# Performance work log

Measured on AMD Instinct MI355X. Metric: run time of the kernel, lower is better.

Reference implementation:

```python
import jax, jax.numpy as jnp
import numpy as np

K, T, RHO, V, TH, EH, S, B = 50, 50, 300, 20000, 800, 200, 10, 256
DELTA = 0.005
LOG_DELTA = float(np.log(DELTA))
EPS = 1e-6


def setup_inputs() -> dict:
    key = jax.random.key(0)
    ks = jax.random.split(key, 32)
    f32 = jnp.float32
    rn = lambda i, shp, s=0.02: jax.random.normal(ks[i], shp, f32) * s
    inp = {
        "unique_tokens": jax.random.randint(ks[0], (100,), 0, V),
        "bows": jax.random.uniform(ks[1], (B, V), f32),
        "normalized_bows": jax.random.uniform(ks[2], (B, V), f32),
        "times": jax.random.randint(ks[3], (B,), 0, T),
        "sources": jax.random.randint(ks[4], (B,), 0, S),
        "rnn_inp": jax.random.normal(ks[5], (S, T, V), f32),
        "num_docs": 100000,
        # learned parameters
        "mu_q_alpha": rn(6, (K, T, RHO), 1.0),
        "logsigma_q_alpha": rn(7, (K, T, RHO), 0.1),
        "rho_W": rn(8, (V, RHO)),                 # Linear(rho_size -> vocab, no bias)
        "W1": rn(9, (TH, V + K)), "b1": jnp.zeros((TH,), f32),
        "W2": rn(10, (TH, TH)), "b2": jnp.zeros((TH,), f32),
        "mu_th_W": rn(11, (K, TH)), "mu_th_b": jnp.zeros((K,), f32),
        "ls_th_W": rn(12, (K, TH)), "ls_th_b": jnp.zeros((K,), f32),
        "eta_map_W": rn(13, (EH, V)), "eta_map_b": jnp.zeros((EH,), f32),
        "lstm_Wih": rn(14, (4 * EH, EH)), "lstm_Whh": rn(15, (4 * EH, EH)),
        "lstm_bih": jnp.zeros((4 * EH,), f32), "lstm_bhh": jnp.zeros((4 * EH,), f32),
        "mu_eta_W": rn(16, (K, EH + K)), "mu_eta_b": jnp.zeros((K,), f32),
        "ls_eta_W": rn(17, (K, EH + K)), "ls_eta_b": jnp.zeros((K,), f32),
        "cls_W": rn(18, (S, K)), "cls_b": jnp.zeros((S,), f32),
    }
    return inp


def _lstm(x_seq, Wih, Whh, bih, bhh):
    # x_seq: [T, S, EH]; torch gate order i,f,g,o
    def step(carry, x):
        h, c = carry
        z = x @ Wih.T + bih + h @ Whh.T + bhh
        i, f, g, o = jnp.split(z, 4, axis=-1)
        c = jax.nn.sigmoid(f) * c + jax.nn.sigmoid(i) * jnp.tanh(g)
        h = jax.nn.sigmoid(o) * jnp.tanh(c)
        return (h, c), h
    h0 = jnp.zeros((x_seq.shape[1], Whh.shape[1]), x_seq.dtype)
    _, out = jax.lax.scan(step, (h0, h0), x_seq)
    return out  # [T, S, EH]


def reference(unique_tokens, bows, normalized_bows, times, sources, rnn_inp, num_docs,
              mu_q_alpha, logsigma_q_alpha, rho_W, W1, b1, W2, b2,
              mu_th_W, mu_th_b, ls_th_W, ls_th_b, eta_map_W, eta_map_b,
              lstm_Wih, lstm_Whh, lstm_bih, lstm_bhh,
              mu_eta_W, mu_eta_b, ls_eta_W, ls_eta_b, cls_W, cls_b):
    # eval-mode semantics: reparameterize returns mu, dropout off
    bsz = bows.shape[0]
    coeff = num_docs / bsz

    # ---- alpha: eval-mode alphas_t == mu_q_alpha[:, t, :]; KL vectorized ----
    mu_a, ls_a = mu_q_alpha, logsigma_q_alpha  # [K, T, RHO]
    kl_a0 = 0.5 * jnp.sum((jnp.exp(ls_a[:, 0]) + mu_a[:, 0] ** 2) / (1.0 + EPS) - 1.0 - ls_a[:, 0])
    diff = mu_a[:, 1:] - mu_a[:, :-1]
    kl_at = 0.5 * jnp.sum((jnp.exp(ls_a[:, 1:]) + diff ** 2) / (DELTA + EPS) - 1.0 + LOG_DELTA - ls_a[:, 1:])
    kl_alpha = kl_a0 + kl_at
    alphas = jnp.transpose(mu_a, (1, 0, 2))  # [T, K, RHO]

    # ---- eta: LSTM over time (vmapped over sources as batch), then recurrence ----
    mapped = jnp.einsum('stv,hv->sth', rnn_inp, eta_map_W) + eta_map_b  # [S, T, EH]
    lstm_out = _lstm(jnp.transpose(mapped, (1, 0, 2)), lstm_Wih, lstm_Whh, lstm_bih, lstm_bhh)  # [T, S, EH]

    inp0 = jnp.concatenate([lstm_out[0], jnp.zeros((S, K), lstm_out.dtype)], axis=-1)
    mu0 = inp0 @ mu_eta_W.T + mu_eta_b
    ls0 = inp0 @ ls_eta_W.T + ls_eta_b  # no clipping at t=0 in original
    kl0 = 0.5 * jnp.sum((jnp.exp(ls0) + mu0 ** 2) / (1.0 + EPS) - 1.0 - ls0)

    def eta_step(carry, out_t):
        eta_prev, kl = carry
        inp_t = jnp.concatenate([out_t, eta_prev], axis=-1)
        mu_t = inp_t @ mu_eta_W.T + mu_eta_b
        ls_t = jnp.clip(inp_t @ ls_eta_W.T + ls_eta_b, -10.0, 10.0)
        kl_t = 0.5 * jnp.sum((jnp.exp(ls_t) + (mu_t - eta_prev) ** 2) / (DELTA + EPS) - 1.0 + LOG_DELTA - ls_t)
        return (mu_t, kl + kl_t), mu_t
    (_, kl_rest), etas_rest = jax.lax.scan(eta_step, (mu0, jnp.float32(0.0)), lstm_out[1:])
    etas = jnp.transpose(jnp.concatenate([mu0[None], etas_rest], axis=0), (1, 0, 2))  # [S, T, K]
    kl_eta = kl0 + kl_rest

    # ---- theta ----
    eta_std = etas[sources, times]  # [B, K]
    h = jax.nn.relu(jnp.concatenate([normalized_bows, eta_std], axis=1) @ W1.T + b1)
    h = jax.nn.relu(h @ W2.T + b2)
    mu_t = h @ mu_th_W.T + mu_th_b
    ls_t = jnp.clip(h @ ls_th_W.T + ls_th_b, -10.0, 10.0)
    theta = jax.nn.softmax(mu_t, axis=-1)
    kl_theta = (0.5 * jnp.sum((jnp.exp(ls_t) + (mu_t - eta_std) ** 2) / (1.0 + EPS) - 1.0 - ls_t)) * coeff

    # ---- beta and NLL ----
    logit = jnp.einsum('tkr,vr->tkv', alphas, rho_W)
    beta = jax.nn.softmax(logit, axis=-1)        # [T, K, V]
    beta_d = beta[times]                         # [B, K, V]
    loglik = jnp.log(jnp.einsum('bk,bkv->bv', theta, beta_d))
    nll = -jnp.sum(loglik * bows) * coeff

    # ---- source prediction loss (sum-reduced cross entropy) ----
    logits = theta @ cls_W.T + cls_b
    logp = jax.nn.log_softmax(logits, axis=-1)
    pred_loss = -jnp.sum(jnp.take_along_axis(logp, sources[:, None], axis=1)) * coeff

    nelbo = nll + kl_alpha + kl_eta + kl_theta + pred_loss
    return (nelbo, nll, kl_alpha, kl_eta, kl_theta, pred_loss)
```

## Files before the change

kernel.cpp:

```cpp
#include <hip/hip_runtime.h>

typedef unsigned int u32;
typedef unsigned short ushort_t;

#define NTOP 50
#define NT_T 50
#define NRHO 300
#define NVOC 20000
#define NTH 800
#define NEH 200
#define NSRC 10
#define NBAT 256

#define OFF_SCAL     0
#define OFF_MAPPED   16
#define OFF_HPRE     100016
#define OFF_H2       304816
#define OFF_Z        509616
#define OFF_DOCCNT   512120
#define OFF_DOCLIST  512176
#define MEMSET_BYTES ((size_t)524976 * 4)
#define OFF_XW       524976
#define OFF_BIAS2    924976
#define OFF_ETAS     925776
#define OFF_WCOEF    950776
#define OFF_W1E      963576
#define OFF_WHH_H    1003576
#define OFF_ETAWH    1083576
#define OFF_H1B      1096080
#define OFF_MAPB     1198480
#define OFF_WIHB     1255824
#define OFF_W2B      1356176
#define OFF_ALPHAB   1714576
#define OFF_RHOB     2124176
#define OFF_NBB      5339536
#define OFF_W1B      7899536
#define OFF_RNNB     16859536
#define OFF_EMWB     21979536
#define OFF_LOGITH   7899536

typedef _Float16 h2v __attribute__((ext_vector_type(2)));
typedef __bf16 bf16x8 __attribute__((ext_vector_type(8)));
typedef float f32x4 __attribute__((ext_vector_type(4)));

__device__ inline float dot2u(u32 a, u32 b, float c){
  h2v ha = __builtin_bit_cast(h2v, a), hb = __builtin_bit_cast(h2v, b);
#if __has_builtin(__builtin_amdgcn_fdot2)
  return __builtin_amdgcn_fdot2(ha, hb, c, false);
#else
  return c + (float)ha.x*(float)hb.x + (float)ha.y*(float)hb.y;
#endif
}

__device__ inline u32 packh2(float lo, float hi){
  h2v h; h.x = (_Float16)lo; h.y = (_Float16)hi;
  return __builtin_bit_cast(u32, h);
}

__device__ inline ushort_t f2bf(float f){
  u32 u = __builtin_bit_cast(u32, f);
  u = (u + 0x7FFFu + ((u >> 16) & 1u)) >> 16;
  return (ushort_t)u;
}

__device__ inline float fast_sig(float x){ return 1.f/(1.f + __expf(-x)); }
__device__ inline float fast_tanh(float x){ float e = __expf(2.f*x); return 1.f - 2.f/(e + 1.f); }

__device__ __forceinline__ void gl2lds16(const void* g, void* l){
  __builtin_amdgcn_global_load_lds((__attribute__((address_space(1))) void*)g,
                                   (__attribute__((address_space(3))) void*)l,
                                   16, 0, 0);
}

__device__ inline void blockReduceAdd(float v, float* red, float* target){
  int tid = threadIdx.x;
  red[tid] = v; __syncthreads();
  for (int o = blockDim.x >> 1; o > 0; o >>= 1){
    if (tid < o) red[tid] += red[tid + o];
    __syncthreads();
  }
  if (tid == 0) atomicAdd(target, red[0]);
}

__global__ __launch_bounds__(256) void k_prep(
    const float* __restrict__ whh,
    const float* __restrict__ muEW, const float* __restrict__ lsEW,
    const float* __restrict__ bih, const float* __restrict__ bhh,
    const float* __restrict__ wih, const float* __restrict__ emapB,
    const float* __restrict__ W1, const int* __restrict__ times,
    float* __restrict__ W)
{
  int idx = blockIdx.x*256 + threadIdx.x;
  u32* whhH = (u32*)(W + OFF_WHH_H);
  u32* etaWH = (u32*)(W + OFF_ETAWH);
  float* bias2 = W + OFF_BIAS2;
  float* w1e = W + OFF_W1E;
  int* docCnt = (int*)(W + OFF_DOCCNT);
  int* docList = (int*)(W + OFF_DOCLIST);
  if (idx < 80000){
    int j = idx/100; int i = idx - j*100;
    whhH[idx] = packh2(whh[j*200 + 2*i], whh[j*200 + 2*i + 1]);
  } else if (idx < 92500){
    int d = idx - 80000; int q = d/125; int i = d - q*125;
    const float* src = (q < 50) ? (muEW + q*250) : (lsEW + (q-50)*250);
    etaWH[d] = packh2(src[2*i], src[2*i+1]);
  } else if (idx < 93300){
    int j = idx - 92500;
    float acc = bih[j] + bhh[j];
    const float* wr = wih + (size_t)j*200;
    #pragma unroll 4
    for (int k = 0; k < 200; k++) acc += emapB[k]*wr[k];
    bias2[j] = acc;
  } else if (idx < 133300){
    int d = idx - 93300; int j = d/50; int k = d - j*50;
    w1e[d] = W1[(size_t)j*20050 + 20000 + k];
  } else if (idx < 133556){
    int b = idx - 133300; int t = times[b];
    int pos = atomicAdd(&docCnt[t], 1);
    docList[t*256 + pos] = b;
  }
}

__global__ __launch_bounds__(256) void k_conv(const float* __restrict__ src, int ldsrc,
                                              int Mreal, int Kused,
                                              ushort_t* __restrict__ dst, int Mp, int Kp)
{
  int idx = blockIdx.x*256 + threadIdx.x;
  int kb = Kp >> 3;
  if (idx >= Mp*kb) return;
  int row = idx / kb, c = (idx - row*kb) << 3;
  ushort_t out[8];
  #pragma unroll
  for (int j = 0; j < 8; j++){
    float v = 0.f;
    int k = c + j;
    if (row < Mreal && k < Kused) v = src[(size_t)row*ldsrc + k];
    out[j] = f2bf(v);
  }
  *(uint4*)(dst + (size_t)row*Kp + c) = *(uint4*)out;
}

__global__ __launch_bounds__(256) void k_conva(const float* __restrict__ muq, ushort_t* __restrict__ dst)
{
  int idx = blockIdx.x*256 + threadIdx.x;
  if (idx >= 2560*40) return;
  int row = idx / 40, c = (idx - row*40) << 3;
  ushort_t out[8];
  const float* src = nullptr;
  if (row < 2500){ int t = row/50, k = row - t*50; src = muq + (size_t)k*15000 + t*300; }
  #pragma unroll
  for (int j = 0; j < 8; j++){
    int r = c + j;
    float v = (src && r < 300) ? src[r] : 0.f;
    out[j] = f2bf(v);
  }
  *(uint4*)(dst + (size_t)row*320 + c) = *(uint4*)out;
}

template<int MODE>
__global__ __launch_bounds__(256) void mfma_nt(
    const ushort_t* __restrict__ A, int lda,
    const ushort_t* __restrict__ B, int ldb,
    float* __restrict__ C, _Float16* __restrict__ Ch, int ldc,
    const float* __restrict__ nBias,
    int M, int N, int mT, int kS, int chunks)
{
  __shared__ __align__(16) ushort_t As[128*32];
  __shared__ __align__(16) ushort_t Bs[128*32];
  int bid = blockIdx.x;
  int kIdx = bid % kS; int rest = bid / kS;
  int mIdx = rest % mT; int nIdx = rest / mT;
  int tid = threadIdx.x;
  int w = tid >> 6, l = tid & 63;
  int c0 = (int)(((long long)chunks * kIdx) / kS);
  int c1 = (int)(((long long)chunks * (kIdx+1)) / kS);
  int r0 = w*32;
  const ushort_t* ga0 = A + (size_t)(mIdx*128 + r0      + (l>>2))*lda + (l&3)*8;
  const ushort_t* ga1 = A + (size_t)(mIdx*128 + r0 + 16 + (l>>2))*lda + (l&3)*8;
  const ushort_t* gb0 = B + (size_t)(nIdx*128 + r0      + (l>>2))*ldb + (l&3)*8;
  const ushort_t* gb1 = B + (size_t)(nIdx*128 + r0 + 16 + (l>>2))*ldb + (l&3)*8;
  ushort_t* la = As + r0*32;
  ushort_t* lb = Bs + r0*32;
  int wr = (w >> 1)*64, wc = (w & 1)*64;
  int lr = l & 15, lq = l >> 4;
  f32x4 acc[4][4];
  #pragma unroll
  for (int i = 0; i < 4; i++)
    #pragma unroll
    for (int j = 0; j < 4; j++)
      acc[i][j] = (f32x4)0.f;

  for (int c = c0; c < c1; c++){
    size_t ko = (size_t)c * 32;
    gl2lds16(ga0 + ko, la);
    gl2lds16(ga1 + ko, la + 512);
    gl2lds16(gb0 + ko, lb);
    gl2lds16(gb1 + ko, lb + 512);
    __syncthreads();
    bf16x8 av[4], bv[4];
    #pragma unroll
    for (int i = 0; i < 4; i++)
      av[i] = *(const bf16x8*)(As + (wr + i*16 + lr)*32 + lq*8);
    #pragma unroll
    for (int j = 0; j < 4; j++)
      bv[j] = *(const bf16x8*)(Bs + (wc + j*16 + lr)*32 + lq*8);
    #pragma unroll
    for (int i = 0; i < 4; i++)
      #pragma unroll
      for (int j = 0; j < 4; j++)
        acc[i][j] = __builtin_amdgcn_mfma_f32_16x16x32_bf16(av[i], bv[j], acc[i][j], 0, 0, 0);
    __syncthreads();
  }
  if (MODE == 3){
    float* Z = C;
    #pragma unroll
    for (int i = 0; i < 4; i++){
      #pragma unroll
      for (int r = 0; r < 4; r++){
        int row = mIdx*128 + wr + i*16 + lq*4 + r;
        float p = 0.f;
        if (row < M){
          #pragma unroll
          for (int j = 0; j < 4; j++){
            int col = nIdx*128 + wc + j*16 + lr;
            if (col < N){
              float e = __expf(acc[i][j][r]);
              Ch[(size_t)row*ldc + col] = (_Float16)e;
              p += e;
            }
          }
        }
        p += __shfl_xor(p, 1, 16);
        p += __shfl_xor(p, 2, 16);
        p += __shfl_xor(p, 4, 16);
        p += __shfl_xor(p, 8, 16);
        if (lr == 0 && row < M) atomicAdd(&Z[row], p);
      }
    }
  } else {
    #pragma unroll
    for (int i = 0; i < 4; i++){
      #pragma unroll
      for (int r = 0; r < 4; r++){
        int row = mIdx*128 + wr + i*16 + lq*4 + r;
        if (row >= M) continue;
        #pragma unroll
        for (int j = 0; j < 4; j++){
          int col = nIdx*128 + wc + j*16 + lr;
          if (col >= N) continue;
          float v = acc[i][j][r];
          if (MODE == 0)      atomicAdd(&C[(size_t)row*ldc + col], v);
          else                C[(size_t)row*ldc + col] = v + nBias[col];
        }
      }
    }
  }
}

__global__ __launch_bounds__(256) void k_klalpha(const float* __restrict__ muq,
                                                 const float* __restrict__ lsq,
                                                 float* __restrict__ W)
{
  __shared__ float red[256];
  const float inv_dl = 1.f/(0.005f + 1e-6f);
  const float logdl = -5.2983173665480363f;
  float local = 0.f;
  for (int idx = blockIdx.x*256 + threadIdx.x; idx < 750000; idx += gridDim.x*256){
    int rem = idx % 15000; int t = rem / 300;
    float ls = lsq[idx]; float mu = muq[idx];
    if (t == 0){
      local += 0.5f*((__expf(ls) + mu*mu)/(1.f + 1e-6f) - 1.f - ls);
    } else {
      float d = mu - muq[idx - 300];
      local += 0.5f*((__expf(ls) + d*d)*inv_dl - 1.f + logdl - ls);
    }
  }
  blockReduceAdd(local, red, W + OFF_SCAL + 1);
}

__global__ __launch_bounds__(512, 2) void k_lstm(
    const float* __restrict__ xw, const u32* __restrict__ whhH, const u32* __restrict__ etaWH,
    const float* __restrict__ muEB, const float* __restrict__ lsEB,
    float* __restrict__ etas, float* __restrict__ W)
{
  int s = blockIdx.x; int tid = threadIdx.x;
  __shared__ uint4 hp4[32];
  __shared__ float zbuf[800];
  __shared__ float red[512];
  u32 wreg[200];
  #pragma unroll
  for (int i = 0; i < 200; i++) wreg[i] = 0u;
  if (tid < 400){
    const u32* ra = whhH + tid*100;
    const u32* rb = whhH + (tid + 400)*100;
    #pragma unroll
    for (int i = 0; i < 100; i++){ wreg[i] = ra[i]; wreg[100+i] = rb[i]; }
  } else if (tid < 500){
    int q = tid - 400;
    const u32* re = etaWH + q*125;
    #pragma unroll
    for (int i = 0; i < 125; i++) wreg[i] = re[i];
  }
  float ebias = 0.f;
  if (tid >= 400 && tid < 500){
    int q = tid - 400;
    ebias = (q < 50) ? muEB[q] : lsEB[q - 50];
  }
  float creg = 0.f, muPrev = 0.f, klLocal = 0.f;
  if (tid < 32){ uint4 z; z.x=z.y=z.z=z.w=0u; hp4[tid] = z; }
  __syncthreads();
  const float inv_dl = 1.f/(0.005f + 1e-6f);
  const float logdl = -5.2983173665480363f;
  _Float16* hview = (_Float16*)hp4;

  for (int t = 0; t < NT_T; t++){
    if (tid < 400){
      float a0=0.f,a1=0.f,a2=0.f,a3=0.f,b0=0.f,b1=0.f,b2=0.f,b3=0.f;
      #pragma unroll
      for (int i4 = 0; i4 < 25; i4++){
        uint4 h = hp4[i4];
        a0 = dot2u(wreg[i4*4+0], h.x, a0);
        a1 = dot2u(wreg[i4*4+1], h.y, a1);
        a2 = dot2u(wreg[i4*4+2], h.z, a2);
        a3 = dot2u(wreg[i4*4+3], h.w, a3);
        b0 = dot2u(wreg[100+i4*4+0], h.x, b0);
        b1 = dot2u(wreg[100+i4*4+1], h.y, b1);
        b2 = dot2u(wreg[100+i4*4+2], h.z, b2);
        b3 = dot2u(wreg[100+i4*4+3], h.w, b3);
      }
      const float* xr = xw + (size_t)(s*50 + t)*800;
      zbuf[tid]       = ((a0+a1)+(a2+a3)) + xr[tid];
      zbuf[tid + 400] = ((b0+b1)+(b2+b3)) + xr[tid + 400];
    }
    __syncthreads();
    if (tid < 200){
      float zi = zbuf[tid], zf = zbuf[200+tid], zg = zbuf[400+tid], zo = zbuf[600+tid];
      float ig = fast_sig(zi);
      float fg = fast_sig(zf);
      float gg = fast_tanh(zg);
      float og = fast_sig(zo);
      creg = fg*creg + ig*gg;
      float hv = og*fast_tanh(creg);
      hview[tid] = (_Float16)hv;
    }
    __syncthreads();
    float eacc = 0.f;
    bool isEta = (tid >= 400 && tid < 500);
    if (isEta){
      float e0=ebias, e1=0.f, e2=0.f, e3=0.f;
      #pragma unroll
      for (int i4 = 0; i4 < 32; i4++){
        uint4 h = hp4[i4];
        e0 = dot2u(wreg[i4*4+0], h.x, e0);
        e1 = dot2u(wreg[i4*4+1], h.y, e1);
        e2 = dot2u(wreg[i4*4+2], h.z, e2);
        e3 = dot2u(wreg[i4*4+3], h.w, e3);
      }
      eacc = (e0+e1)+(e2+e3);
    }
    __syncthreads();
    if (isEta){
      int q = tid - 400;
      if (q < 50){
        float mu = eacc;
        etas[(size_t)(s*50 + t)*50 + q] = mu;
        if (t == 0) klLocal += 0.5f*mu*mu/(1.f + 1e-6f);
        else { float d = mu - muPrev; klLocal += 0.5f*d*d*inv_dl; }
        muPrev = mu;
        hview[200 + q] = (_Float16)mu;
      } else {
        float ls = eacc;
        if (t == 0) klLocal += 0.5f*(__expf(ls)/(1.f + 1e-6f) - 1.f - ls);
        else {
          ls = fminf(fmaxf(ls, -10.f), 10.f);
          klLocal += 0.5f*(__expf(ls)*inv_dl - 1.f + logdl - ls);
        }
      }
    }
  }
  __syncthreads();
  blockReduceAdd(klLocal, red, W + OFF_SCAL + 2);
}

__global__ __launch_bounds__(256) void k_h1(
    const float* __restrict__ hpre, const float* __restrict__ b1, const float* __restrict__ w1e,
    const float* __restrict__ etas, const int* __restrict__ times, const int* __restrict__ srcs,
    ushort_t* __restrict__ h1B)
{
  int b = blockIdx.x, tid = threadIdx.x;
  __shared__ float et[50];
  int tb = times[b], sb = srcs[b];
  if (tid < 50) et[tid] = etas[(size_t)(sb*50 + tb)*50 + tid];
  __syncthreads();
  for (int j = tid; j < 800; j += 256){
    float acc = hpre[(size_t)b*800 + j] + b1[j];
    const float* wrow = w1e + (size_t)j*50;
    #pragma unroll
    for (int k = 0; k < 50; k++) acc += et[k]*wrow[k];
    h1B[(size_t)b*800 + j] = f2bf(fmaxf(acc, 0.f));
  }
}

__global__ __launch_bounds__(256) void k_thfin(
    const float* __restrict__ h2g, const float* __restrict__ b2, const float* __restrict__ etas,
    const int* __restrict__ times, const int* __restrict__ srcs,
    const float* __restrict__ muW, const float* __restrict__ muB,
    const float* __restrict__ lsW, const float* __restrict__ lsB,
    const float* __restrict__ clsW, const float* __restrict__ clsB,
    const float* __restrict__ Zrow, float* __restrict__ wcoef, float* __restrict__ W)
{
  int b = blockIdx.x, tid = threadIdx.x;
  __shared__ float h2s[800], mu[50], lsv[50], et[50], th[50], lg[10], red[64], shm[2];
  for (int j = tid; j < 800; j += 256) h2s[j] = fmaxf(h2g[(size_t)b*800 + j] + b2[j], 0.f);
  int tb = times[b], sb = srcs[b];
  if (tid < 50) et[tid] = etas[(size_t)(sb*50 + tb)*50 + tid];
  __syncthreads();
  if (tid < 100){
    int q = (tid < 50) ? tid : tid - 50;
    const float* w = (tid < 50) ? (muW + (size_t)q*800) : (lsW + (size_t)q*800);
    float acc = (tid < 50) ? muB[q] : lsB[q];
    #pragma unroll 8
    for (int j = 0; j < 800; j++) acc += h2s[j]*w[j];
    if (tid < 50) mu[q] = acc;
    else lsv[q] = fminf(fmaxf(acc, -10.f), 10.f);
  }
  __syncthreads();
  if (tid == 0){ float m = -1e30f; for (int k = 0; k < 50; k++) m = fmaxf(m, mu[k]); shm[0] = m; }
  __syncthreads();
  if (tid < 50) th[tid] = __expf(mu[tid] - shm[0]);
  __syncthreads();
  if (tid == 0){ float z = 0.f; for (int k = 0; k < 50; k++) z += th[k]; shm[1] = z; }
  __syncthreads();
  if (tid < 64) red[tid] = 0.f;
  if (tid < 50){
    float t_ = th[tid]/shm[1]; th[tid] = t_;
    wcoef[(size_t)b*50 + tid] = t_/Zrow[tb*50 + tid];
    float d = mu[tid] - et[tid];
    red[tid] = 0.5f*((__expf(lsv[tid]) + d*d)/(1.f + 1e-6f) - 1.f - lsv[tid]);
  }
  __syncthreads();
  if (tid < 10){
    float a = clsB[tid];
    #pragma unroll
    for (int k = 0; k < 50; k++) a += th[k]*clsW[tid*50 + k];
    lg[tid] = a;
  }
  __syncthreads();
  if (tid == 0){
    float m = -1e30f; for (int i = 0; i < 10; i++) m = fmaxf(m, lg[i]);
    float z = 0.f; for (int i = 0; i < 10; i++) z += __expf(lg[i] - m);
    float lse = m + __logf(z);
    atomicAdd(W + OFF_SCAL + 4, lse - lg[sb]);
    float ssum = 0.f; for (int i = 0; i < 50; i++) ssum += red[i];
    atomicAdd(W + OFF_SCAL + 3, ssum);
  }
}

__global__ __launch_bounds__(256) void k_nll(
    const _Float16* __restrict__ E, const float* __restrict__ wcoef,
    const float* __restrict__ bows, float* __restrict__ W)
{
  int t = blockIdx.x/10, vc = blockIdx.x%10;
  int v0 = vc*2000;
  int tid = threadIdx.x;
  const int* docCnt = (const int*)(W + OFF_DOCCNT);
  const int* docList = (const int*)(W + OFF_DOCLIST);
  __shared__ float wch[64*50];
  __shared__ int ids[64];
  __shared__ float red[256];
  int nd = docCnt[t];
  float acc = 0.f;
  for (int d0 = 0; d0 < nd; d0 += 64){
    int ndc = min(64, nd - d0);
    __syncthreads();
    for (int i = tid; i < ndc*50; i += 256){
      int d = i/50, k = i - d*50;
      int bb = docList[t*256 + d0 + d];
      if (k == 0) ids[d] = bb;
      wch[i] = wcoef[(size_t)bb*50 + k];
    }
    __syncthreads();
    for (int v = v0 + tid; v < v0 + 2000; v += 256){
      float e[50];
      #pragma unroll
      for (int k = 0; k < 50; k++)
        e[k] = (float)E[(size_t)(t*50 + k)*NVOC + v];
      for (int d = 0; d < ndc; d++){
        float s = 0.f;
        #pragma unroll
        for (int k = 0; k < 50; k++) s += wch[d*50 + k]*e[k];
        acc += bows[(size_t)ids[d]*NVOC + v]*__logf(s);
      }
    }
  }
  __syncthreads();
  blockReduceAdd(acc, red, W + OFF_SCAL + 0);
}

__global__ void k_final(const float* __restrict__ W, const int* __restrict__ ndocs, float* __restrict__ out)
{
  if (blockIdx.x == 0 && threadIdx.x == 0){
    float coeff = (float)ndocs[0] / 256.f;
    const float* scal = W + OFF_SCAL;
    float nll  = -scal[0]*coeff;
    float kla  = scal[1];
    float kle  = scal[2];
    float klth = scal[3]*coeff;
    float pred = scal[4]*coeff;
    out[0] = nll + kla + kle + klth + pred;
    out[1] = nll; out[2] = kla; out[3] = kle; out[4] = klth; out[5] = pred;
  }
}

extern "C" void kernel_launch(void* const* d_in, const int* in_sizes, int n_in,
                              void* d_out, int out_size, void* d_ws, size_t ws_size,
                              hipStream_t stream)
{
  (void)in_sizes; (void)n_in; (void)out_size; (void)ws_size;
  const float* bows  = (const float*)d_in[1];
  const float* nb    = (const float*)d_in[2];
  const int*   times = (const int*)d_in[3];
  const int*   srcs  = (const int*)d_in[4];
  const float* rnn   = (const float*)d_in[5];
  const int*   ndocs = (const int*)d_in[6];
  const float* muq   = (const float*)d_in[7];
  const float* lsq   = (const float*)d_in[8];
  const float* rho   = (const float*)d_in[9];
  const float* W1    = (const float*)d_in[10];
  const float* b1    = (const float*)d_in[11];
  const float* W2    = (const float*)d_in[12];
  const float* b2    = (const float*)d_in[13];
  const float* muthW = (const float*)d_in[14];
  const float* muthB = (const float*)d_in[15];
  const float* lsthW = (const float*)d_in[16];
  const float* lsthB = (const float*)d_in[17];
  const float* emapW = (const float*)d_in[18];
  const float* emapB = (const float*)d_in[19];
  const float* wih   = (const float*)d_in[20];
  const float* whh   = (const float*)d_in[21];
  const float* bih   = (const float*)d_in[22];
  const float* bhh   = (const float*)d_in[23];
  const float* muEW  = (const float*)d_in[24];
  const float* muEB  = (const float*)d_in[25];
  const float* lsEW  = (const float*)d_in[26];
  const float* lsEB  = (const float*)d_in[27];
  const float* clsW  = (const float*)d_in[28];
  const float* clsB  = (const float*)d_in[29];

  float* W = (float*)d_ws;
  ushort_t* alphaB = (ushort_t*)(W + OFF_ALPHAB);
  ushort_t* rhoB   = (ushort_t*)(W + OFF_RHOB);
  ushort_t* nbB    = (ushort_t*)(W + OFF_NBB);
  ushort_t* w1B    = (ushort_t*)(W + OFF_W1B);
  ushort_t* rnnB   = (ushort_t*)(W + OFF_RNNB);
  ushort_t* emwB   = (ushort_t*)(W + OFF_EMWB);
  ushort_t* wihB   = (ushort_t*)(W + OFF_WIHB);
  ushort_t* w2B    = (ushort_t*)(W + OFF_W2B);
  ushort_t* mapB   = (ushort_t*)(W + OFF_MAPB);
  ushort_t* h1B    = (ushort_t*)(W + OFF_H1B);
  _Float16* Ehalf  = (_Float16*)(W + OFF_LOGITH);

  hipMemsetAsync(d_ws, 0, MEMSET_BYTES, stream);

  k_prep<<<522, 256, 0, stream>>>(whh, muEW, lsEW, bih, bhh, wih, emapB, W1, times, W);

  k_conva<<<400, 256, 0, stream>>>(muq, alphaB);
  k_conv<<<3140, 256, 0, stream>>>(rho, 300, 20000, 300, rhoB, 20096, 320);
  k_conv<<<2500, 256, 0, stream>>>(nb, 20000, 256, 20000, nbB, 256, 20000);
  k_conv<<<8750, 256, 0, stream>>>(W1, 20050, 800, 20000, w1B, 896, 20000);
  k_conv<<<5000, 256, 0, stream>>>(rnn, 20000, 500, 20000, rnnB, 512, 20000);
  k_conv<<<2500, 256, 0, stream>>>(emapW, 20000, 200, 20000, emwB, 256, 20000);
  k_conv<<<98, 256, 0, stream>>>(wih, 200, 800, 200, wihB, 896, 224);
  k_conv<<<350, 256, 0, stream>>>(W2, 800, 800, 800, w2B, 896, 800);

  mfma_nt<0><<<4*2*32, 256, 0, stream>>>(
      rnnB, 20000, emwB, 20000, W + OFF_MAPPED, nullptr, 200, nullptr,
      500, 200, 4, 32, 625);

  mfma_nt<0><<<2*7*20, 256, 0, stream>>>(
      nbB, 20000, w1B, 20000, W + OFF_HPRE, nullptr, 800, nullptr,
      256, 800, 2, 20, 625);

  mfma_nt<3><<<20*157, 256, 0, stream>>>(
      alphaB, 320, rhoB, 320, W + OFF_Z, Ehalf, 20000, nullptr,
      2500, 20000, 20, 1, 10);

  k_conv<<<56, 256, 0, stream>>>(W + OFF_MAPPED, 200, 500, 200, mapB, 512, 224);

  mfma_nt<2><<<4*7, 256, 0, stream>>>(
      mapB, 224, wihB, 224, W + OFF_XW, nullptr, 800, W + OFF_BIAS2,
      500, 800, 4, 1, 7);

  k_klalpha<<<1024, 256, 0, stream>>>(muq, lsq, W);

  k_lstm<<<NSRC, 512, 0, stream>>>(W + OFF_XW, (const u32*)(W + OFF_WHH_H),
                                   (const u32*)(W + OFF_ETAWH), muEB, lsEB,
                                   W + OFF_ETAS, W);

  k_h1<<<256, 256, 0, stream>>>(W + OFF_HPRE, b1, W + OFF_W1E, W + OFF_ETAS, times, srcs, h1B);

  mfma_nt<0><<<2*7*2, 256, 0, stream>>>(
      h1B, 800, w2B, 800, W + OFF_H2, nullptr, 800, nullptr,
      256, 800, 2, 2, 25);

  k_thfin<<<256, 256, 0, stream>>>(W + OFF_H2, b2, W + OFF_ETAS, times, srcs,
                                   muthW, muthB, lsthW, lsthB, clsW, clsB,
                                   W + OFF_Z, W + OFF_WCOEF, W);

  k_nll<<<500, 256, 0, stream>>>(Ehalf, W + OFF_WCOEF, bows, W);

  k_final<<<1, 64, 0, stream>>>(W, ndocs, (float*)d_out);
}
```

Measured before the change: 733.9 us.

## Fuse prep, conversion and KL-alpha kernels into one launch; double-buffer LSTM hidden state

Merges the prep, all bf16 conversion kernels and the KL-alpha reduction into a single large kernel that dispatches work by block index, replacing ten launches with one. The LSTM now keeps its weights in named uint4 registers instead of an indexed array, and pads the eta weights to 128 entries per row so they can be loaded as uint4. It also double-buffers the hidden-state shared buffer, which removes one __syncthreads per timestep because the eta projection reads the new h and the previous eta half from separate buffers. The risks are higher register pressure and a heavier branchy mega-kernel.

```diff
diff --git a/kernel.cpp b/kernel.cpp
--- a/kernel.cpp
+++ b/kernel.cpp
@@ -27,21 +27,25 @@
 #define OFF_W1E      963576
 #define OFF_WHH_H    1003576
 #define OFF_ETAWH    1083576
-#define OFF_H1B      1096080
-#define OFF_MAPB     1198480
-#define OFF_WIHB     1255824
-#define OFF_W2B      1356176
-#define OFF_ALPHAB   1714576
-#define OFF_RHOB     2124176
-#define OFF_NBB      5339536
-#define OFF_W1B      7899536
-#define OFF_RNNB     16859536
-#define OFF_EMWB     21979536
-#define OFF_LOGITH   7899536
+#define OFF_H1B      1096376
+#define OFF_MAPB     1198776
+#define OFF_WIHB     1256120
+#define OFF_W2B      1356472
+#define OFF_ALPHAB   1714872
+#define OFF_RHOB     2124472
+#define OFF_NBB      5339832
+#define OFF_W1B      7899832
+#define OFF_RNNB     16859832
+#define OFF_EMWB     21979832
+#define OFF_LOGITH   7899832
 
 typedef _Float16 h2v __attribute__((ext_vector_type(2)));
 typedef __bf16 bf16x8 __attribute__((ext_vector_type(8)));
 typedef float f32x4 __attribute__((ext_vector_type(4)));
+
+#define REP25(M) M(0) M(1) M(2) M(3) M(4) M(5) M(6) M(7) M(8) M(9) M(10) M(11) M(12) \
+                 M(13) M(14) M(15) M(16) M(17) M(18) M(19) M(20) M(21) M(22) M(23) M(24)
+#define REP7(M) M(0) M(1) M(2) M(3) M(4) M(5) M(6)
 
 __device__ inline float dot2u(u32 a, u32 b, float c){
   h2v ha = __builtin_bit_cast(h2v, a), hb = __builtin_bit_cast(h2v, b);
@@ -82,52 +86,11 @@
   if (tid == 0) atomicAdd(target, red[0]);
 }
 
-__global__ __launch_bounds__(256) void k_prep(
-    const float* __restrict__ whh,
-    const float* __restrict__ muEW, const float* __restrict__ lsEW,
-    const float* __restrict__ bih, const float* __restrict__ bhh,
-    const float* __restrict__ wih, const float* __restrict__ emapB,
-    const float* __restrict__ W1, const int* __restrict__ times,
-    float* __restrict__ W)
-{
-  int idx = blockIdx.x*256 + threadIdx.x;
-  u32* whhH = (u32*)(W + OFF_WHH_H);
-  u32* etaWH = (u32*)(W + OFF_ETAWH);
-  float* bias2 = W + OFF_BIAS2;
-  float* w1e = W + OFF_W1E;
-  int* docCnt = (int*)(W + OFF_DOCCNT);
-  int* docList = (int*)(W + OFF_DOCLIST);
-  if (idx < 80000){
-    int j = idx/100; int i = idx - j*100;
-    whhH[idx] = packh2(whh[j*200 + 2*i], whh[j*200 + 2*i + 1]);
-  } else if (idx < 92500){
-    int d = idx - 80000; int q = d/125; int i = d - q*125;
-    const float* src = (q < 50) ? (muEW + q*250) : (lsEW + (q-50)*250);
-    etaWH[d] = packh2(src[2*i], src[2*i+1]);
-  } else if (idx < 93300){
-    int j = idx - 92500;
-    float acc = bih[j] + bhh[j];
-    const float* wr = wih + (size_t)j*200;
-    #pragma unroll 4
-    for (int k = 0; k < 200; k++) acc += emapB[k]*wr[k];
-    bias2[j] = acc;
-  } else if (idx < 133300){
-    int d = idx - 93300; int j = d/50; int k = d - j*50;
-    w1e[d] = W1[(size_t)j*20050 + 20000 + k];
-  } else if (idx < 133556){
-    int b = idx - 133300; int t = times[b];
-    int pos = atomicAdd(&docCnt[t], 1);
-    docList[t*256 + pos] = b;
-  }
-}
-
-__global__ __launch_bounds__(256) void k_conv(const float* __restrict__ src, int ldsrc,
-                                              int Mreal, int Kused,
-                                              ushort_t* __restrict__ dst, int Mp, int Kp)
-{
-  int idx = blockIdx.x*256 + threadIdx.x;
+__device__ inline void conv_seg(const float* __restrict__ src, int ldsrc,
+                                int Mreal, int Kused,
+                                ushort_t* __restrict__ dst, int Kp, int idx)
+{
   int kb = Kp >> 3;
-  if (idx >= Mp*kb) return;
   int row = idx / kb, c = (idx - row*kb) << 3;
   ushort_t out[8];
   #pragma unroll
@@ -140,21 +103,104 @@
   *(uint4*)(dst + (size_t)row*Kp + c) = *(uint4*)out;
 }
 
-__global__ __launch_bounds__(256) void k_conva(const float* __restrict__ muq, ushort_t* __restrict__ dst)
+__global__ __launch_bounds__(256) void k_mega(
+    const float* __restrict__ whh,
+    const float* __restrict__ muEW, const float* __restrict__ lsEW,
+    const float* __restrict__ bih, const float* __restrict__ bhh,
+    const float* __restrict__ wih, const float* __restrict__ emapB,
+    const float* __restrict__ W1, const int* __restrict__ times,
+    const float* __restrict__ muq, const float* __restrict__ lsq,
+    const float* __restrict__ rho, const float* __restrict__ nb,
+    const float* __restrict__ rnn, const float* __restrict__ emapW,
+    const float* __restrict__ W2f, float* __restrict__ W)
+{
+  int b = blockIdx.x, tid = threadIdx.x;
+  __shared__ float red[256];
+  if (b < 523){
+    int idx = b*256 + tid;
+    u32* whhH = (u32*)(W + OFF_WHH_H);
+    u32* etaWH = (u32*)(W + OFF_ETAWH);
+    if (idx < 80000){
+      int j = idx/100; int i = idx - j*100;
+      whhH[idx] = packh2(whh[j*200 + 2*i], whh[j*200 + 2*i + 1]);
+    } else if (idx < 92800){
+      int d = idx - 80000; int q = d >> 7; int i = d & 127;
+      u32 v = 0u;
+      if (i < 125){
+        const float* src = (q < 50) ? (muEW + q*250) : (lsEW + (q-50)*250);
+        v = packh2(src[2*i], src[2*i+1]);
+      }
+      etaWH[d] = v;
+    } else if (idx < 93600){
+      int j = idx - 92800;
+      float acc = bih[j] + bhh[j];
+      const float* wr = wih + (size_t)j*200;
+      #pragma unroll 4
+      for (int k = 0; k < 200; k++) acc += emapB[k]*wr[k];
+      W[OFF_BIAS2 + j] = acc;
+    } else if (idx < 133600){
+      int d = idx - 93600; int j = d/50; int k = d - j*50;
+      W[OFF_W1E + d] = W1[(size_t)j*20050 + 20000 + k];
+    } else if (idx < 133856){
+      int bb = idx - 133600; int t = times[bb];
+      int* docCnt = (int*)(W + OFF_DOCCNT);
+      int* docList = (int*)(W + OFF_DOCLIST);
+      int pos = atomicAdd(&docCnt[t], 1);
+      docList[t*256 + pos] = bb;
+    }
+  } else if (b < 923){
+    int idx = (b-523)*256 + tid;
+    int row = idx / 40, c = (idx - row*40) << 3;
+    ushort_t out[8];
+    const float* src = nullptr;
+    if (row < 2500){ int t = row/50, k = row - t*50; src = muq + (size_t)k*15000 + t*300; }
+    #pragma unroll
+    for (int j = 0; j < 8; j++){
+      int r = c + j;
+      float v = (src && r < 300) ? src[r] : 0.f;
+      out[j] = f2bf(v);
+    }
+    *(uint4*)((ushort_t*)(W + OFF_ALPHAB) + (size_t)row*320 + c) = *(uint4*)out;
+  } else if (b < 4063){
+    conv_seg(rho, 300, 20000, 300, (ushort_t*)(W + OFF_RHOB), 320, (b-923)*256 + tid);
+  } else if (b < 6563){
+    conv_seg(nb, 20000, 256, 20000, (ushort_t*)(W + OFF_NBB), 20000, (b-4063)*256 + tid);
+  } else if (b < 15313){
+    conv_seg(W1, 20050, 800, 20000, (ushort_t*)(W + OFF_W1B), 20000, (b-6563)*256 + tid);
+  } else if (b < 20313){
+    conv_seg(rnn, 20000, 500, 20000, (ushort_t*)(W + OFF_RNNB), 20000, (b-15313)*256 + tid);
+  } else if (b < 22813){
+    conv_seg(emapW, 20000, 200, 20000, (ushort_t*)(W + OFF_EMWB), 20000, (b-20313)*256 + tid);
+  } else if (b < 22911){
+    conv_seg(wih, 200, 800, 200, (ushort_t*)(W + OFF_WIHB), 224, (b-22813)*256 + tid);
+  } else if (b < 23261){
+    conv_seg(W2f, 800, 800, 800, (ushort_t*)(W + OFF_W2B), 800, (b-22911)*256 + tid);
+  } else {
+    const float inv_dl = 1.f/(0.005f + 1e-6f);
+    const float logdl = -5.2983173665480363f;
+    float local = 0.f;
+    for (int idx = (b-23261)*256 + tid; idx < 750000; idx += 1024*256){
+      int rem = idx % 15000; int t = rem / 300;
+      float ls = lsq[idx]; float mu = muq[idx];
+      if (t == 0){
+        local += 0.5f*((__expf(ls) + mu*mu)/(1.f + 1e-6f) - 1.f - ls);
+      } else {
+        float d = mu - muq[idx - 300];
+        local += 0.5f*((__expf(ls) + d*d)*inv_dl - 1.f + logdl - ls);
+      }
+    }
+    blockReduceAdd(local, red, W + OFF_SCAL + 1);
+  }
+}
+
+__global__ __launch_bounds__(256) void k_conv(const float* __restrict__ src, int ldsrc,
+                                              int Mreal, int Kused,
+                                              ushort_t* __restrict__ dst, int Mp, int Kp)
 {
   int idx = blockIdx.x*256 + threadIdx.x;
-  if (idx >= 2560*40) return;
-  int row = idx / 40, c = (idx - row*40) << 3;
-  ushort_t out[8];
-  const float* src = nullptr;
-  if (row < 2500){ int t = row/50, k = row - t*50; src = muq + (size_t)k*15000 + t*300; }
-  #pragma unroll
-  for (int j = 0; j < 8; j++){
-    int r = c + j;
-    float v = (src && r < 300) ? src[r] : 0.f;
-    out[j] = f2bf(v);
-  }
-  *(uint4*)(dst + (size_t)row*320 + c) = *(uint4*)out;
+  int kb = Kp >> 3;
+  if (idx >= Mp*kb) return;
+  conv_seg(src, ldsrc, Mreal, Kused, dst, Kp, idx);
 }
 
 template<int MODE>
@@ -257,77 +303,55 @@
   }
 }
 
-__global__ __launch_bounds__(256) void k_klalpha(const float* __restrict__ muq,
-                                                 const float* __restrict__ lsq,
-                                                 float* __restrict__ W)
-{
-  __shared__ float red[256];
+__global__ __launch_bounds__(512, 2) void k_lstm(
+    const float* __restrict__ xw, const u32* __restrict__ whhH, const uint4* __restrict__ etaW4,
+    const float* __restrict__ muEB, const float* __restrict__ lsEB,
+    float* __restrict__ etas, float* __restrict__ W)
+{
+  int s = blockIdx.x; int tid = threadIdx.x;
+  __shared__ uint4 hp4[2][32];
+  __shared__ float zbuf[800];
+  __shared__ float red[512];
+  uint4 z4; z4.x = z4.y = z4.z = z4.w = 0u;
+#define DECLW(i) uint4 wa##i = z4, wb##i = z4;
+  REP25(DECLW)
+#undef DECLW
+  float ebias = 0.f;
+  if (tid < 400){
+    const uint4* ra = (const uint4*)(whhH + tid*100);
+    const uint4* rb = (const uint4*)(whhH + (tid + 400)*100);
+#define LDW(i) wa##i = ra[i]; wb##i = rb[i];
+    REP25(LDW)
+#undef LDW
+  } else if (tid < 500){
+    int q = tid - 400;
+    const uint4* re = etaW4 + q*32;
+#define LDA(i) wa##i = re[i];
+    REP25(LDA)
+#undef LDA
+#define LDB(i) wb##i = re[25+i];
+    REP7(LDB)
+#undef LDB
+    ebias = (q < 50) ? muEB[q] : lsEB[q - 50];
+  }
+  float creg = 0.f, muPrev = 0.f, klLocal = 0.f;
+  if (tid < 64) ((uint4*)hp4)[tid] = z4;
+  __syncthreads();
   const float inv_dl = 1.f/(0.005f + 1e-6f);
   const float logdl = -5.2983173665480363f;
-  float local = 0.f;
-  for (int idx = blockIdx.x*256 + threadIdx.x; idx < 750000; idx += gridDim.x*256){
-    int rem = idx % 15000; int t = rem / 300;
-    float ls = lsq[idx]; float mu = muq[idx];
-    if (t == 0){
-      local += 0.5f*((__expf(ls) + mu*mu)/(1.f + 1e-6f) - 1.f - ls);
-    } else {
-      float d = mu - muq[idx - 300];
-      local += 0.5f*((__expf(ls) + d*d)*inv_dl - 1.f + logdl - ls);
-    }
-  }
-  blockReduceAdd(local, red, W + OFF_SCAL + 1);
-}
-
-__global__ __launch_bounds__(512, 2) void k_lstm(
-    const float* __restrict__ xw, const u32* __restrict__ whhH, const u32* __restrict__ etaWH,
-    const float* __restrict__ muEB, const float* __restrict__ lsEB,
-    float* __restrict__ etas, float* __restrict__ W)
-{
-  int s = blockIdx.x; int tid = threadIdx.x;
-  __shared__ uint4 hp4[32];
-  __shared__ float zbuf[800];
-  __shared__ float red[512];
-  u32 wreg[200];
-  #pragma unroll
-  for (int i = 0; i < 200; i++) wreg[i] = 0u;
-  if (tid < 400){
-    const u32* ra = whhH + tid*100;
-    const u32* rb = whhH + (tid + 400)*100;
-    #pragma unroll
-    for (int i = 0; i < 100; i++){ wreg[i] = ra[i]; wreg[100+i] = rb[i]; }
-  } else if (tid < 500){
-    int q = tid - 400;
-    const u32* re = etaWH + q*125;
-    #pragma unroll
-    for (int i = 0; i < 125; i++) wreg[i] = re[i];
-  }
-  float ebias = 0.f;
-  if (tid >= 400 && tid < 500){
-    int q = tid - 400;
-    ebias = (q < 50) ? muEB[q] : lsEB[q - 50];
-  }
-  float creg = 0.f, muPrev = 0.f, klLocal = 0.f;
-  if (tid < 32){ uint4 z; z.x=z.y=z.z=z.w=0u; hp4[tid] = z; }
-  __syncthreads();
-  const float inv_dl = 1.f/(0.005f + 1e-6f);
-  const float logdl = -5.2983173665480363f;
-  _Float16* hview = (_Float16*)hp4;
 
   for (int t = 0; t < NT_T; t++){
+    const uint4* hc = hp4[t & 1];
+    uint4* hn = hp4[(t + 1) & 1];
     if (tid < 400){
       float a0=0.f,a1=0.f,a2=0.f,a3=0.f,b0=0.f,b1=0.f,b2=0.f,b3=0.f;
-      #pragma unroll
-      for (int i4 = 0; i4 < 25; i4++){
-        uint4 h = hp4[i4];
-        a0 = dot2u(wreg[i4*4+0], h.x, a0);
-        a1 = dot2u(wreg[i4*4+1], h.y, a1);
-        a2 = dot2u(wreg[i4*4+2], h.z, a2);
-        a3 = dot2u(wreg[i4*4+3], h.w, a3);
-        b0 = dot2u(wreg[100+i4*4+0], h.x, b0);
-        b1 = dot2u(wreg[100+i4*4+1], h.y, b1);
-        b2 = dot2u(wreg[100+i4*4+2], h.z, b2);
-        b3 = dot2u(wreg[100+i4*4+3], h.w, b3);
-      }
+#define DOT(i) { uint4 h = hc[i]; \
+      a0 = dot2u(wa##i.x, h.x, a0); a1 = dot2u(wa##i.y, h.y, a1); \
+      a2 = dot2u(wa##i.z, h.z, a2); a3 = dot2u(wa##i.w, h.w, a3); \
+      b0 = dot2u(wb##i.x, h.x, b0); b1 = dot2u(wb##i.y, h.y, b1); \
+      b2 = dot2u(wb##i.z, h.z, b2); b3 = dot2u(wb##i.w, h.w, b3); }
+      REP25(DOT)
+#undef DOT
       const float* xr = xw + (size_t)(s*50 + t)*800;
       zbuf[tid]       = ((a0+a1)+(a2+a3)) + xr[tid];
       zbuf[tid + 400] = ((b0+b1)+(b2+b3)) + xr[tid + 400];
@@ -341,25 +365,22 @@
       float og = fast_sig(zo);
       creg = fg*creg + ig*gg;
       float hv = og*fast_tanh(creg);
-      hview[tid] = (_Float16)hv;
+      ((_Float16*)hn)[tid] = (_Float16)hv;
     }
     __syncthreads();
-    float eacc = 0.f;
-    bool isEta = (tid >= 400 && tid < 500);
-    if (isEta){
-      float e0=ebias, e1=0.f, e2=0.f, e3=0.f;
-      #pragma unroll
-      for (int i4 = 0; i4 < 32; i4++){
-        uint4 h = hp4[i4];
-        e0 = dot2u(wreg[i4*4+0], h.x, e0);
-        e1 = dot2u(wreg[i4*4+1], h.y, e1);
-        e2 = dot2u(wreg[i4*4+2], h.z, e2);
-        e3 = dot2u(wreg[i4*4+3], h.w, e3);
-      }
-      eacc = (e0+e1)+(e2+e3);
-    }
-    __syncthreads();
-    if (isEta){
+    if (tid >= 400 && tid < 500){
+      float e0 = ebias, e1 = 0.f, e2 = 0.f, e3 = 0.f;
+#define DOTE(i) { uint4 h = hn[i]; \
+      e0 = dot2u(wa##i.x, h.x, e0); e1 = dot2u(wa##i.y, h.y, e1); \
+      e2 = dot2u(wa##i.z, h.z, e2); e3 = dot2u(wa##i.w, h.w, e3); }
+      REP25(DOTE)
+#undef DOTE
+#define DOTP(i) { uint4 h = hc[25+i]; \
+      e0 = dot2u(wb##i.x, h.x, e0); e1 = dot2u(wb##i.y, h.y, e1); \
+      e2 = dot2u(wb##i.z, h.z, e2); e3 = dot2u(wb##i.w, h.w, e3); }
+      REP7(DOTP)
+#undef DOTP
+      float eacc = (e0+e1)+(e2+e3);
       int q = tid - 400;
       if (q < 50){
         float mu = eacc;
@@ -367,7 +388,7 @@
         if (t == 0) klLocal += 0.5f*mu*mu/(1.f + 1e-6f);
         else { float d = mu - muPrev; klLocal += 0.5f*d*d*inv_dl; }
         muPrev = mu;
-        hview[200 + q] = (_Float16)mu;
+        ((_Float16*)hn)[200 + q] = (_Float16)mu;
       } else {
         float ls = eacc;
         if (t == 0) klLocal += 0.5f*(__expf(ls)/(1.f + 1e-6f) - 1.f - ls);
@@ -562,16 +583,8 @@
 
   hipMemsetAsync(d_ws, 0, MEMSET_BYTES, stream);
 
-  k_prep<<<522, 256, 0, stream>>>(whh, muEW, lsEW, bih, bhh, wih, emapB, W1, times, W);
-
-  k_conva<<<400, 256, 0, stream>>>(muq, alphaB);
-  k_conv<<<3140, 256, 0, stream>>>(rho, 300, 20000, 300, rhoB, 20096, 320);
-  k_conv<<<2500, 256, 0, stream>>>(nb, 20000, 256, 20000, nbB, 256, 20000);
-  k_conv<<<8750, 256, 0, stream>>>(W1, 20050, 800, 20000, w1B, 896, 20000);
-  k_conv<<<5000, 256, 0, stream>>>(rnn, 20000, 500, 20000, rnnB, 512, 20000);
-  k_conv<<<2500, 256, 0, stream>>>(emapW, 20000, 200, 20000, emwB, 256, 20000);
-  k_conv<<<98, 256, 0, stream>>>(wih, 200, 800, 200, wihB, 896, 224);
-  k_conv<<<350, 256, 0, stream>>>(W2, 800, 800, 800, w2B, 896, 800);
+  k_mega<<<24285, 256, 0, stream>>>(whh, muEW, lsEW, bih, bhh, wih, emapB, W1, times,
+                                    muq, lsq, rho, nb, rnn, emapW, W2, W);
 
   mfma_nt<0><<<4*2*32, 256, 0, stream>>>(
       rnnB, 20000, emwB, 20000, W + OFF_MAPPED, nullptr, 200, nullptr,
@@ -591,10 +604,8 @@
       mapB, 224, wihB, 224, W + OFF_XW, nullptr, 800, W + OFF_BIAS2,
       500, 800, 4, 1, 7);
 
-  k_klalpha<<<1024, 256, 0, stream>>>(muq, lsq, W);
-
   k_lstm<<<NSRC, 512, 0, stream>>>(W + OFF_XW, (const u32*)(W + OFF_WHH_H),
-                                   (const u32*)(W + OFF_ETAWH), muEB, lsEB,
+                                   (const uint4*)(W + OFF_ETAWH), muEB, lsEB,
                                    W + OFF_ETAS, W);
 
   k_h1<<<256, 256, 0, stream>>>(W + OFF_HPRE, b1, W + OFF_W1E, W + OFF_ETAS, times, srcs, h1B);
```

Measured after the change: 712.0 us. 1.03x faster.
